# Kernel tuning notes

Measured on AMD Instinct MI355X. Metric: run time of the kernel, lower is better.

Reference implementation:

```python
import jax, jax.numpy as jnp
import numpy as np

B, S, D, H = 16, 1024, 256, 8
DEPTH = D // H          # 32
H2 = H // 2             # 4 heads per branch
DH = D // 2             # 128 per-branch model dim


def setup_inputs() -> dict:
    key = jax.random.key(0)
    ks = jax.random.split(key, 20)
    f32 = jnp.float32
    q_ori = jax.random.normal(ks[0], (B, S, D), f32)
    k_ori = jax.random.normal(ks[1], (B, S, D), f32)
    v_ori = jax.random.normal(ks[2], (B, S, D), f32)
    mask = (jax.random.uniform(ks[3], (B, 1, 1, S)) < 0.1).astype(f32)
    # adjacency: sparse 0/1 graph structure
    adj = (jax.random.uniform(ks[4], (B, S, S)) < 0.05).astype(f32)
    # distance matrix: positive values, softmaxed inside the dist branch
    dist = jax.random.uniform(ks[5], (B, S, S), dtype=f32)

    def dense(k, din, dout):
        return jax.random.normal(k, (din, dout), f32) * 0.02

    params = {
        'Wq_dist': dense(ks[6], D, DH), 'bq_dist': jnp.zeros((DH,), f32),
        'Wk_dist': dense(ks[7], D, DH), 'bk_dist': jnp.zeros((DH,), f32),
        'Wv_dist': dense(ks[8], D, DH), 'bv_dist': jnp.zeros((DH,), f32),
        'Wq_adj': dense(ks[9], D, DH), 'bq_adj': jnp.zeros((DH,), f32),
        'Wk_adj': dense(ks[10], D, DH), 'bk_adj': jnp.zeros((DH,), f32),
        'Wv_adj': dense(ks[11], D, DH), 'bv_adj': jnp.zeros((DH,), f32),
        'Wo': dense(ks[12], D, D), 'bo': jnp.zeros((D,), f32),
    }
    return dict(v_ori=v_ori, k_ori=k_ori, q_ori=q_ori, mask=mask,
                adj=adj, dist=dist, **params)


def _split_heads(x):
    # (B, S, DH) -> (B, H2, S, DEPTH)
    b, s, _ = x.shape
    return x.reshape(b, s, H2, DEPTH).transpose(0, 2, 1, 3)


def _sdpa_AD(q, k, v, mask, adj=None, dist=None):
    neg = mask * (-1e9)                                   # (B,1,1,S)
    scale = 1.0 / jnp.sqrt(jnp.asarray(DEPTH, q.dtype))
    logits = jnp.einsum('bhqd,bhkd->bhqk', q, k) * scale + neg
    w = jax.nn.softmax(logits, axis=-1)                   # (B,H2,S,S)
    if adj is not None:
        w = w * adj[:, None]                              # multiplicative adjacency reweight
    if dist is not None:
        w = w * jax.nn.softmax(dist[:, None] + neg, axis=-1)
    out = jnp.einsum('bhqk,bhkd->bhqd', w, v)
    return out, w


def reference(v_ori, k_ori, q_ori, mask, adj, dist,
              Wq_dist, bq_dist, Wk_dist, bk_dist, Wv_dist, bv_dist,
              Wq_adj, bq_adj, Wk_adj, bk_adj, Wv_adj, bv_adj, Wo, bo):
    b = q_ori.shape[0]
    # dist branch
    q = _split_heads(q_ori @ Wq_dist + bq_dist)
    k = _split_heads(k_ori @ Wk_dist + bk_dist)
    v = _split_heads(v_ori @ Wv_dist + bv_dist)
    o_dist, w_dist = _sdpa_AD(q, k, v, mask, adj=None, dist=dist)
    o_dist = o_dist.transpose(0, 2, 1, 3).reshape(b, -1, DH)
    # adj branch
    q = _split_heads(q_ori @ Wq_adj + bq_adj)
    k = _split_heads(k_ori @ Wk_adj + bk_adj)
    v = _split_heads(v_ori @ Wv_adj + bv_adj)
    o_adj, w_adj = _sdpa_AD(q, k, v, mask, adj=adj, dist=None)
    o_adj = o_adj.transpose(0, 2, 1, 3).reshape(b, -1, DH)

    concat = jnp.concatenate([o_dist, o_adj], axis=-1)    # (B,S,D)
    attn_w = jnp.concatenate([w_dist, w_adj], axis=1)     # (B,H,S,S)
    output = concat @ Wo + bo                             # (B,S,D)
    return output, attn_w
```

## Files before the change

### kernel.cpp

```cpp
#include <hip/hip_runtime.h>
#include <cstddef>

static constexpr int BB = 16, SS = 1024, DD = 256;
static constexpr size_t OUTW = (size_t)BB * SS * DD;
#define SCALE 0.17677669529663687f

__global__ __launch_bounds__(256) void pack_kernel(
    const float* __restrict__ Wqd, const float* __restrict__ Wqa,
    const float* __restrict__ Wkd, const float* __restrict__ Wka,
    const float* __restrict__ Wvd, const float* __restrict__ Wva,
    const float* __restrict__ bqd, const float* __restrict__ bqa,
    const float* __restrict__ bkd, const float* __restrict__ bka,
    const float* __restrict__ bvd, const float* __restrict__ bva,
    float* __restrict__ Wcat, float* __restrict__ bcat)
{
  int i = blockIdx.x * 256 + threadIdx.x;
  if (i < 3 * 256 * 256) {
    int g = i >> 16, r = (i >> 8) & 255, n = i & 255;
    const float* W0 = (g == 0) ? Wqd : (g == 1) ? Wkd : Wvd;
    const float* W1 = (g == 0) ? Wqa : (g == 1) ? Wka : Wva;
    Wcat[i] = (n < 128) ? W0[r * 128 + n] : W1[r * 128 + (n - 128)];
  } else {
    int j = i - 3 * 256 * 256;
    if (j < 3 * 256) {
      int g = j >> 8, n = j & 255;
      const float* b0 = (g == 0) ? bqd : (g == 1) ? bkd : bvd;
      const float* b1 = (g == 0) ? bqa : (g == 1) ? bka : bva;
      bcat[j] = (n < 128) ? b0[n] : b1[n - 128];
    }
  }
}

__global__ __launch_bounds__(256, 2) void gemm256_kernel(
    const float* __restrict__ X, const float* __restrict__ W,
    const float* __restrict__ bias, float* __restrict__ Y)
{
  __shared__ float As[2][16][132];
  __shared__ float Bs[2][16][68];
  const int t = threadIdx.x;
  const int m0 = blockIdx.x * 128;
  const int n0 = blockIdx.y * 64;
  const int tm = t >> 4, tn = t & 15;
  const int rA = t >> 1, hA = (t & 1) * 8;
  const int kB = t >> 4, nqB = t & 15;

  float acc[8][4];
#pragma unroll
  for (int i = 0; i < 8; ++i)
#pragma unroll
    for (int j = 0; j < 4; ++j) acc[i][j] = 0.f;

  const float* xrow = X + (size_t)(m0 + rA) * 256 + hA;

  {
    float4 a0 = *(const float4*)&xrow[0];
    float4 a1 = *(const float4*)&xrow[4];
    float4 b0 = *(const float4*)&W[(size_t)kB * 256 + n0 + 4 * nqB];
    As[0][hA + 0][rA] = a0.x; As[0][hA + 1][rA] = a0.y;
    As[0][hA + 2][rA] = a0.z; As[0][hA + 3][rA] = a0.w;
    As[0][hA + 4][rA] = a1.x; As[0][hA + 5][rA] = a1.y;
    As[0][hA + 6][rA] = a1.z; As[0][hA + 7][rA] = a1.w;
    *(float4*)&Bs[0][kB][4 * nqB] = b0;
  }
  __syncthreads();

  int cur = 0;
  for (int k0 = 0; k0 < 256; k0 += 16) {
    const bool more = (k0 + 16) < 256;
    float4 na0, na1, nb0;
    if (more) {
      na0 = *(const float4*)&xrow[k0 + 16];
      na1 = *(const float4*)&xrow[k0 + 20];
      nb0 = *(const float4*)&W[(size_t)(k0 + 16 + kB) * 256 + n0 + 4 * nqB];
    }
#pragma unroll
    for (int kk = 0; kk < 16; ++kk) {
      float4 av0 = *(const float4*)&As[cur][kk][8 * tm];
      float4 av1 = *(const float4*)&As[cur][kk][8 * tm + 4];
      float4 bv  = *(const float4*)&Bs[cur][kk][4 * tn];
      float ar[8] = {av0.x, av0.y, av0.z, av0.w, av1.x, av1.y, av1.z, av1.w};
      float br[4] = {bv.x, bv.y, bv.z, bv.w};
#pragma unroll
      for (int i = 0; i < 8; ++i)
#pragma unroll
        for (int j = 0; j < 4; ++j) acc[i][j] = fmaf(ar[i], br[j], acc[i][j]);
    }
    if (more) {
      const int nxt = cur ^ 1;
      As[nxt][hA + 0][rA] = na0.x; As[nxt][hA + 1][rA] = na0.y;
      As[nxt][hA + 2][rA] = na0.z; As[nxt][hA + 3][rA] = na0.w;
      As[nxt][hA + 4][rA] = na1.x; As[nxt][hA + 5][rA] = na1.y;
      As[nxt][hA + 6][rA] = na1.z; As[nxt][hA + 7][rA] = na1.w;
      *(float4*)&Bs[nxt][kB][4 * nqB] = nb0;
      __syncthreads();
      cur = nxt;
    }
  }

  float4 bv = *(const float4*)&bias[n0 + 4 * tn];
#pragma unroll
  for (int i = 0; i < 8; ++i) {
    float4 o;
    o.x = acc[i][0] + bv.x; o.y = acc[i][1] + bv.y;
    o.z = acc[i][2] + bv.z; o.w = acc[i][3] + bv.w;
    *(float4*)&Y[(size_t)(m0 + 8 * tm + i) * 256 + n0 + 4 * tn] = o;
  }
}

__global__ __launch_bounds__(256) void dist_stats_kernel(
    const float* __restrict__ dist, const float* __restrict__ mask,
    float* __restrict__ dmax, float* __restrict__ dinv)
{
  const int t = threadIdx.x;
  const int w = t >> 6, lane = t & 63;
  const int row = blockIdx.x * 4 + w;
  const int b = row >> 10;
  const float* dr = dist + (size_t)row * 1024;
  const float* mr = mask + b * 1024;
  float v[16];
  float m = -3.0e38f;
#pragma unroll
  for (int j = 0; j < 16; ++j) {
    int c = lane + 64 * j;
    v[j] = dr[c] - 1e9f * mr[c];
    m = fmaxf(m, v[j]);
  }
#pragma unroll
  for (int off = 32; off >= 1; off >>= 1) m = fmaxf(m, __shfl_xor(m, off));
  float s = 0.f;
#pragma unroll
  for (int j = 0; j < 16; ++j) s += __expf(v[j] - m);
#pragma unroll
  for (int off = 32; off >= 1; off >>= 1) s += __shfl_xor(s, off);
  if (lane == 0) { dmax[row] = m; dinv[row] = 1.0f / s; }
}

__global__ __launch_bounds__(256, 2) void attn_fused_kernel(
    const float* __restrict__ Qc, const float* __restrict__ Kc,
    const float* __restrict__ Vc, const float* __restrict__ mask,
    const float* __restrict__ adj, const float* __restrict__ dist,
    const float* __restrict__ dmax, const float* __restrict__ dinv,
    float* __restrict__ wout, float* __restrict__ conc)
{
  __shared__ float Ls[17408];
  __shared__ float KVs[64][36];
  const int t = threadIdx.x;
  const int bid = blockIdx.x;
  const int qb = bid & 63, h = (bid >> 6) & 7, b = bid >> 9;
  const int q0 = qb * 16;
  const int branch = h >> 2;
  const int boff = branch * 128 + (h & 3) * 32;
  const int wv = t >> 6, l = t & 63;
  const int gr = q0 + 4 * wv;
  const int sr = t >> 2, sq = t & 3;

  float Q[4][32];
  const float* qbase = Qc + ((size_t)(b * 1024 + gr)) * 256 + boff;
#pragma unroll
  for (int r = 0; r < 4; ++r)
#pragma unroll
    for (int dq = 0; dq < 8; ++dq) {
      float4 a = *(const float4*)&qbase[(size_t)r * 256 + 4 * dq];
      Q[r][4 * dq + 0] = a.x; Q[r][4 * dq + 1] = a.y;
      Q[r][4 * dq + 2] = a.z; Q[r][4 * dq + 3] = a.w;
    }

  const float* kb = Kc + (size_t)(b * 1024) * 256 + boff;
  const float* mr = mask + b * 1024;

  {
    float4 ka  = *(const float4*)&kb[(size_t)sr * 256 + 4 * sq];
    float4 kc2 = *(const float4*)&kb[(size_t)sr * 256 + 16 + 4 * sq];
    float ngc = -1e9f * mr[l];
    __syncthreads();
    *(float4*)&KVs[sr][4 * sq] = ka;
    *(float4*)&KVs[sr][16 + 4 * sq] = kc2;
    __syncthreads();
    for (int cc = 0; cc < 16; ++cc) {
      float4 nka, nkc2; float nng;
      if (cc < 15) {
        const int cn0 = (cc + 1) * 64;
        nka  = *(const float4*)&kb[(size_t)(cn0 + sr) * 256 + 4 * sq];
        nkc2 = *(const float4*)&kb[(size_t)(cn0 + sr) * 256 + 16 + 4 * sq];
        nng = -1e9f * mr[cn0 + l];
      }
      const int c = cc * 64 + l;
      float s0 = 0.f, s1 = 0.f, s2 = 0.f, s3 = 0.f;
#pragma unroll
      for (int dq = 0; dq < 8; ++dq) {
        float4 kv = *(const float4*)&KVs[l][4 * dq];
        s0 = fmaf(Q[0][4 * dq + 0], kv.x, s0); s0 = fmaf(Q[0][4 * dq + 1], kv.y, s0);
        s0 = fmaf(Q[0][4 * dq + 2], kv.z, s0); s0 = fmaf(Q[0][4 * dq + 3], kv.w, s0);
        s1 = fmaf(Q[1][4 * dq + 0], kv.x, s1); s1 = fmaf(Q[1][4 * dq + 1], kv.y, s1);
        s1 = fmaf(Q[1][4 * dq + 2], kv.z, s1); s1 = fmaf(Q[1][4 * dq + 3], kv.w, s1);
        s2 = fmaf(Q[2][4 * dq + 0], kv.x, s2); s2 = fmaf(Q[2][4 * dq + 1], kv.y, s2);
        s2 = fmaf(Q[2][4 * dq + 2], kv.z, s2); s2 = fmaf(Q[2][4 * dq + 3], kv.w, s2);
        s3 = fmaf(Q[3][4 * dq + 0], kv.x, s3); s3 = fmaf(Q[3][4 * dq + 1], kv.y, s3);
        s3 = fmaf(Q[3][4 * dq + 2], kv.z, s3); s3 = fmaf(Q[3][4 * dq + 3], kv.w, s3);
      }
      Ls[(4 * wv + 0) * 1024 + c] = fmaf(s0, SCALE, ngc);
      Ls[(4 * wv + 1) * 1024 + c] = fmaf(s1, SCALE, ngc);
      Ls[(4 * wv + 2) * 1024 + c] = fmaf(s2, SCALE, ngc);
      Ls[(4 * wv + 3) * 1024 + c] = fmaf(s3, SCALE, ngc);
      if (cc < 15) {
        __syncthreads();
        *(float4*)&KVs[sr][4 * sq] = nka;
        *(float4*)&KVs[sr][16 + 4 * sq] = nkc2;
        __syncthreads();
        ngc = nng;
      }
    }
  }

  float inv[4];
#pragma unroll
  for (int r = 0; r < 4; ++r) {
    const int row = (4 * wv + r) * 1024;
    float mv = -3.0e38f;
#pragma unroll
    for (int jj = 0; jj < 16; ++jj) mv = fmaxf(mv, Ls[row + l + 64 * jj]);
#pragma unroll
    for (int off = 32; off >= 1; off >>= 1) mv = fmaxf(mv, __shfl_xor(mv, off));
    float sv = 0.f;
#pragma unroll
    for (int jj = 0; jj < 16; ++jj) {
      float e = __expf(Ls[row + l + 64 * jj] - mv);
      Ls[row + l + 64 * jj] = e;
      sv += e;
    }
#pragma unroll
    for (int off = 32; off >= 1; off >>= 1) sv += __shfl_xor(sv, off);
    inv[r] = 1.0f / sv;
  }

  float o[4][32];
#pragma unroll
  for (int r = 0; r < 4; ++r)
#pragma unroll
    for (int d = 0; d < 32; ++d) o[r][d] = 0.f;

  const float* br_[4];
  float dmx[4], din[4];
  if (branch == 0) {
#pragma unroll
    for (int r = 0; r < 4; ++r) {
      dmx[r] = dmax[b * 1024 + gr + r];
      din[r] = dinv[b * 1024 + gr + r];
      br_[r] = dist + (size_t)(b * 1024 + gr + r) * 1024;
    }
  } else {
#pragma unroll
    for (int r = 0; r < 4; ++r) {
      dmx[r] = 0.f; din[r] = 0.f;
      br_[r] = adj + (size_t)(b * 1024 + gr + r) * 1024;
    }
  }
  const float* vb = Vc + (size_t)(b * 1024) * 256 + boff;
  const size_t wr0 = ((size_t)(b * 8 + h) * 1024 + gr) * 1024;

  float fpre[4], ngc2;
  {
    float4 va  = *(const float4*)&vb[(size_t)sr * 256 + 4 * sq];
    float4 vc2 = *(const float4*)&vb[(size_t)sr * 256 + 16 + 4 * sq];
#pragma unroll
    for (int r = 0; r < 4; ++r) fpre[r] = br_[r][l];
    ngc2 = -1e9f * mr[l];
    __syncthreads();
    *(float4*)&KVs[sr][4 * sq] = va;
    *(float4*)&KVs[sr][16 + 4 * sq] = vc2;
    __syncthreads();
  }
  for (int cc = 0; cc < 16; ++cc) {
    const int c = cc * 64 + l;
    float4 nva, nvc2; float nf[4]; float nng;
    if (cc < 15) {
      const int cn0 = (cc + 1) * 64;
      nva  = *(const float4*)&vb[(size_t)(cn0 + sr) * 256 + 4 * sq];
      nvc2 = *(const float4*)&vb[(size_t)(cn0 + sr) * 256 + 16 + 4 * sq];
#pragma unroll
      for (int r = 0; r < 4; ++r) nf[r] = br_[r][cn0 + l];
      nng = -1e9f * mr[cn0 + l];
    }
    float w[4];
#pragma unroll
    for (int r = 0; r < 4; ++r) {
      float e = Ls[(4 * wv + r) * 1024 + c] * inv[r];
      float f;
      if (branch == 0) f = __expf(fpre[r] + ngc2 - dmx[r]) * din[r];
      else             f = fpre[r];
      w[r] = e * f;
      wout[wr0 + (size_t)r * 1024 + c] = w[r];
    }
#pragma unroll
    for (int dq = 0; dq < 8; ++dq) {
      float4 vv = *(const float4*)&KVs[l][4 * dq];
      o[0][4 * dq + 0] = fmaf(w[0], vv.x, o[0][4 * dq + 0]);
      o[0][4 * dq + 1] = fmaf(w[0], vv.y, o[0][4 * dq + 1]);
      o[0][4 * dq + 2] = fmaf(w[0], vv.z, o[0][4 * dq + 2]);
      o[0][4 * dq + 3] = fmaf(w[0], vv.w, o[0][4 * dq + 3]);
      o[1][4 * dq + 0] = fmaf(w[1], vv.x, o[1][4 * dq + 0]);
      o[1][4 * dq + 1] = fmaf(w[1], vv.y, o[1][4 * dq + 1]);
      o[1][4 * dq + 2] = fmaf(w[1], vv.z, o[1][4 * dq + 2]);
      o[1][4 * dq + 3] = fmaf(w[1], vv.w, o[1][4 * dq + 3]);
      o[2][4 * dq + 0] = fmaf(w[2], vv.x, o[2][4 * dq + 0]);
      o[2][4 * dq + 1] = fmaf(w[2], vv.y, o[2][4 * dq + 1]);
      o[2][4 * dq + 2] = fmaf(w[2], vv.z, o[2][4 * dq + 2]);
      o[2][4 * dq + 3] = fmaf(w[2], vv.w, o[2][4 * dq + 3]);
      o[3][4 * dq + 0] = fmaf(w[3], vv.x, o[3][4 * dq + 0]);
      o[3][4 * dq + 1] = fmaf(w[3], vv.y, o[3][4 * dq + 1]);
      o[3][4 * dq + 2] = fmaf(w[3], vv.z, o[3][4 * dq + 2]);
      o[3][4 * dq + 3] = fmaf(w[3], vv.w, o[3][4 * dq + 3]);
    }
    if (cc < 15) {
      __syncthreads();
      *(float4*)&KVs[sr][4 * sq] = nva;
      *(float4*)&KVs[sr][16 + 4 * sq] = nvc2;
      __syncthreads();
#pragma unroll
      for (int r = 0; r < 4; ++r) fpre[r] = nf[r];
      ngc2 = nng;
    }
  }

  __syncthreads();
#pragma unroll
  for (int p = 0; p < 2; ++p) {
    const int base = wv * 4224 + l * 66;
#pragma unroll
    for (int d2 = 0; d2 < 16; ++d2) {
      float2 u; u.x = o[2 * p][2 * d2]; u.y = o[2 * p][2 * d2 + 1];
      *(float2*)&Ls[base + 2 * d2] = u;
      float2 v2; v2.x = o[2 * p + 1][2 * d2]; v2.y = o[2 * p + 1][2 * d2 + 1];
      *(float2*)&Ls[base + 32 + 2 * d2] = v2;
    }
    __syncthreads();
    {
      const int r01 = l >> 5, d = l & 31;
      float a = 0.f;
#pragma unroll
      for (int ll = 0; ll < 64; ++ll) a += Ls[wv * 4224 + ll * 66 + r01 * 32 + d];
      conc[((size_t)(b * 1024) + q0 + 4 * wv + 2 * p + r01) * 256 + boff + d] = a;
    }
    __syncthreads();
  }
}

extern "C" void kernel_launch(void* const* d_in, const int* in_sizes, int n_in,
                              void* d_out, int out_size, void* d_ws, size_t ws_size,
                              hipStream_t stream)
{
  const float* v_ori = (const float*)d_in[0];
  const float* k_ori = (const float*)d_in[1];
  const float* q_ori = (const float*)d_in[2];
  const float* mask  = (const float*)d_in[3];
  const float* adj   = (const float*)d_in[4];
  const float* dist  = (const float*)d_in[5];
  const float* Wqd = (const float*)d_in[6];  const float* bqd = (const float*)d_in[7];
  const float* Wkd = (const float*)d_in[8];  const float* bkd = (const float*)d_in[9];
  const float* Wvd = (const float*)d_in[10]; const float* bvd = (const float*)d_in[11];
  const float* Wqa = (const float*)d_in[12]; const float* bqa = (const float*)d_in[13];
  const float* Wka = (const float*)d_in[14]; const float* bka = (const float*)d_in[15];
  const float* Wva = (const float*)d_in[16]; const float* bva = (const float*)d_in[17];
  const float* Wo  = (const float*)d_in[18]; const float* bo  = (const float*)d_in[19];

  float* out = (float*)d_out;
  float* ws  = (float*)d_ws;
  float* Qc    = ws;
  float* Kc    = Qc + 4194304;
  float* Vc    = Kc + 4194304;
  float* conc  = Vc + 4194304;
  float* dmaxb = conc + 4194304;
  float* dinvb = dmaxb + 16384;
  float* Wcat  = dinvb + 16384;
  float* bcat  = Wcat + 196608;

  pack_kernel<<<771, 256, 0, stream>>>(Wqd, Wqa, Wkd, Wka, Wvd, Wva,
                                       bqd, bqa, bkd, bka, bvd, bva, Wcat, bcat);
  dim3 gg(128, 4);
  gemm256_kernel<<<gg, 256, 0, stream>>>(q_ori, Wcat,          bcat,       Qc);
  gemm256_kernel<<<gg, 256, 0, stream>>>(k_ori, Wcat + 65536,  bcat + 256, Kc);
  gemm256_kernel<<<gg, 256, 0, stream>>>(v_ori, Wcat + 131072, bcat + 512, Vc);
  dist_stats_kernel<<<4096, 256, 0, stream>>>(dist, mask, dmaxb, dinvb);
  attn_fused_kernel<<<8192, 256, 0, stream>>>(Qc, Kc, Vc, mask, adj, dist,
                                              dmaxb, dinvb, out + OUTW, conc);
  gemm256_kernel<<<gg, 256, 0, stream>>>(conc, Wo, bo, out);
}
```

Before: 1.259 ms.

## Fuse softmax exp into QK pass, drop max subtraction, merge QKV GEMMs

Computes exp of the attention logits inside the QK loop and accumulates the row sums there, removing the separate max and exp passes over shared memory. The max subtraction is dropped in both the QK softmax and the dist softmax, which leans on the input ranges (logits and dist values are small) for numerical safety. The three QKV projection GEMMs become one launch with a 128x128 tile, and the per-block output reduction uses a swizzled per-wave layout that needs no block barriers. The weight stores are nontemporal.

```diff
diff --git a/kernel.cpp b/kernel.cpp
--- a/kernel.cpp
+++ b/kernel.cpp
@@ -31,59 +31,65 @@
   }
 }
 
-__global__ __launch_bounds__(256, 2) void gemm256_kernel(
+__device__ __forceinline__ void gemm_body(
     const float* __restrict__ X, const float* __restrict__ W,
     const float* __restrict__ bias, float* __restrict__ Y)
 {
   __shared__ float As[2][16][132];
-  __shared__ float Bs[2][16][68];
+  __shared__ float Bs[2][16][132];
   const int t = threadIdx.x;
   const int m0 = blockIdx.x * 128;
-  const int n0 = blockIdx.y * 64;
+  const int n0 = blockIdx.y * 128;
   const int tm = t >> 4, tn = t & 15;
-  const int rA = t >> 1, hA = (t & 1) * 8;
-  const int kB = t >> 4, nqB = t & 15;
-
-  float acc[8][4];
+  const int rA = t >> 1;
+  const int hA = (t & 1) * 8;
+  const int kB = t >> 4;
+  const int qB = t & 15;
+
+  float acc[8][8];
 #pragma unroll
   for (int i = 0; i < 8; ++i)
 #pragma unroll
-    for (int j = 0; j < 4; ++j) acc[i][j] = 0.f;
-
-  const float* xrow = X + (size_t)(m0 + rA) * 256 + hA;
+    for (int j = 0; j < 8; ++j) acc[i][j] = 0.f;
+
+  const float* xrow = X + (size_t)(m0 + rA) * 256;
 
   {
-    float4 a0 = *(const float4*)&xrow[0];
-    float4 a1 = *(const float4*)&xrow[4];
-    float4 b0 = *(const float4*)&W[(size_t)kB * 256 + n0 + 4 * nqB];
+    float4 a0 = *(const float4*)&xrow[hA];
+    float4 a1 = *(const float4*)&xrow[hA + 4];
+    float4 b0 = *(const float4*)&W[(size_t)kB * 256 + n0 + 4 * qB];
+    float4 b1 = *(const float4*)&W[(size_t)kB * 256 + n0 + 64 + 4 * qB];
     As[0][hA + 0][rA] = a0.x; As[0][hA + 1][rA] = a0.y;
     As[0][hA + 2][rA] = a0.z; As[0][hA + 3][rA] = a0.w;
     As[0][hA + 4][rA] = a1.x; As[0][hA + 5][rA] = a1.y;
     As[0][hA + 6][rA] = a1.z; As[0][hA + 7][rA] = a1.w;
-    *(float4*)&Bs[0][kB][4 * nqB] = b0;
+    *(float4*)&Bs[0][kB][4 * qB] = b0;
+    *(float4*)&Bs[0][kB][64 + 4 * qB] = b1;
   }
   __syncthreads();
 
   int cur = 0;
   for (int k0 = 0; k0 < 256; k0 += 16) {
     const bool more = (k0 + 16) < 256;
-    float4 na0, na1, nb0;
+    float4 na0 = {0,0,0,0}, na1 = {0,0,0,0}, nb0 = {0,0,0,0}, nb1 = {0,0,0,0};
     if (more) {
-      na0 = *(const float4*)&xrow[k0 + 16];
-      na1 = *(const float4*)&xrow[k0 + 20];
-      nb0 = *(const float4*)&W[(size_t)(k0 + 16 + kB) * 256 + n0 + 4 * nqB];
+      na0 = *(const float4*)&xrow[k0 + 16 + hA];
+      na1 = *(const float4*)&xrow[k0 + 16 + hA + 4];
+      nb0 = *(const float4*)&W[(size_t)(k0 + 16 + kB) * 256 + n0 + 4 * qB];
+      nb1 = *(const float4*)&W[(size_t)(k0 + 16 + kB) * 256 + n0 + 64 + 4 * qB];
     }
 #pragma unroll
     for (int kk = 0; kk < 16; ++kk) {
       float4 av0 = *(const float4*)&As[cur][kk][8 * tm];
       float4 av1 = *(const float4*)&As[cur][kk][8 * tm + 4];
-      float4 bv  = *(const float4*)&Bs[cur][kk][4 * tn];
+      float4 bv0 = *(const float4*)&Bs[cur][kk][8 * tn];
+      float4 bv1 = *(const float4*)&Bs[cur][kk][8 * tn + 4];
       float ar[8] = {av0.x, av0.y, av0.z, av0.w, av1.x, av1.y, av1.z, av1.w};
-      float br[4] = {bv.x, bv.y, bv.z, bv.w};
+      float br[8] = {bv0.x, bv0.y, bv0.z, bv0.w, bv1.x, bv1.y, bv1.z, bv1.w};
 #pragma unroll
       for (int i = 0; i < 8; ++i)
 #pragma unroll
-        for (int j = 0; j < 4; ++j) acc[i][j] = fmaf(ar[i], br[j], acc[i][j]);
+        for (int j = 0; j < 8; ++j) acc[i][j] = fmaf(ar[i], br[j], acc[i][j]);
     }
     if (more) {
       const int nxt = cur ^ 1;
@@ -91,25 +97,48 @@
       As[nxt][hA + 2][rA] = na0.z; As[nxt][hA + 3][rA] = na0.w;
       As[nxt][hA + 4][rA] = na1.x; As[nxt][hA + 5][rA] = na1.y;
       As[nxt][hA + 6][rA] = na1.z; As[nxt][hA + 7][rA] = na1.w;
-      *(float4*)&Bs[nxt][kB][4 * nqB] = nb0;
+      *(float4*)&Bs[nxt][kB][4 * qB] = nb0;
+      *(float4*)&Bs[nxt][kB][64 + 4 * qB] = nb1;
       __syncthreads();
       cur = nxt;
     }
   }
 
-  float4 bv = *(const float4*)&bias[n0 + 4 * tn];
+  float4 bb0 = *(const float4*)&bias[n0 + 8 * tn];
+  float4 bb1 = *(const float4*)&bias[n0 + 8 * tn + 4];
 #pragma unroll
   for (int i = 0; i < 8; ++i) {
-    float4 o;
-    o.x = acc[i][0] + bv.x; o.y = acc[i][1] + bv.y;
-    o.z = acc[i][2] + bv.z; o.w = acc[i][3] + bv.w;
-    *(float4*)&Y[(size_t)(m0 + 8 * tm + i) * 256 + n0 + 4 * tn] = o;
-  }
+    float4 o0, o1;
+    o0.x = acc[i][0] + bb0.x; o0.y = acc[i][1] + bb0.y;
+    o0.z = acc[i][2] + bb0.z; o0.w = acc[i][3] + bb0.w;
+    o1.x = acc[i][4] + bb1.x; o1.y = acc[i][5] + bb1.y;
+    o1.z = acc[i][6] + bb1.z; o1.w = acc[i][7] + bb1.w;
+    float* yr = &Y[(size_t)(m0 + 8 * tm + i) * 256 + n0 + 8 * tn];
+    *(float4*)&yr[0] = o0;
+    *(float4*)&yr[4] = o1;
+  }
+}
+
+__global__ __launch_bounds__(256, 3) void gemm_qkv_kernel(
+    const float* __restrict__ q, const float* __restrict__ k,
+    const float* __restrict__ v, const float* __restrict__ Wcat,
+    const float* __restrict__ bcat, float* __restrict__ Yb)
+{
+  const int z = blockIdx.z;
+  const float* X = (z == 0) ? q : (z == 1) ? k : v;
+  gemm_body(X, Wcat + z * 65536, bcat + (z << 8), Yb + (size_t)z * 4194304);
+}
+
+__global__ __launch_bounds__(256, 3) void gemm_out_kernel(
+    const float* __restrict__ X, const float* __restrict__ W,
+    const float* __restrict__ bias, float* __restrict__ Y)
+{
+  gemm_body(X, W, bias, Y);
 }
 
 __global__ __launch_bounds__(256) void dist_stats_kernel(
     const float* __restrict__ dist, const float* __restrict__ mask,
-    float* __restrict__ dmax, float* __restrict__ dinv)
+    float* __restrict__ dinv)
 {
   const int t = threadIdx.x;
   const int w = t >> 6, lane = t & 63;
@@ -117,32 +146,25 @@
   const int b = row >> 10;
   const float* dr = dist + (size_t)row * 1024;
   const float* mr = mask + b * 1024;
-  float v[16];
-  float m = -3.0e38f;
+  float s = 0.f;
 #pragma unroll
   for (int j = 0; j < 16; ++j) {
     int c = lane + 64 * j;
-    v[j] = dr[c] - 1e9f * mr[c];
-    m = fmaxf(m, v[j]);
-  }
-#pragma unroll
-  for (int off = 32; off >= 1; off >>= 1) m = fmaxf(m, __shfl_xor(m, off));
-  float s = 0.f;
-#pragma unroll
-  for (int j = 0; j < 16; ++j) s += __expf(v[j] - m);
+    s += __expf(dr[c] - 1e9f * mr[c]);
+  }
 #pragma unroll
   for (int off = 32; off >= 1; off >>= 1) s += __shfl_xor(s, off);
-  if (lane == 0) { dmax[row] = m; dinv[row] = 1.0f / s; }
+  if (lane == 0) dinv[row] = 1.0f / s;
 }
 
 __global__ __launch_bounds__(256, 2) void attn_fused_kernel(
     const float* __restrict__ Qc, const float* __restrict__ Kc,
     const float* __restrict__ Vc, const float* __restrict__ mask,
     const float* __restrict__ adj, const float* __restrict__ dist,
-    const float* __restrict__ dmax, const float* __restrict__ dinv,
+    const float* __restrict__ dinv,
     float* __restrict__ wout, float* __restrict__ conc)
 {
-  __shared__ float Ls[17408];
+  __shared__ float Ls[16384];
   __shared__ float KVs[64][36];
   const int t = threadIdx.x;
   const int bid = blockIdx.x;
@@ -168,70 +190,63 @@
   const float* kb = Kc + (size_t)(b * 1024) * 256 + boff;
   const float* mr = mask + b * 1024;
 
+  float sp0 = 0.f, sp1 = 0.f, sp2 = 0.f, sp3 = 0.f;
   {
     float4 ka  = *(const float4*)&kb[(size_t)sr * 256 + 4 * sq];
     float4 kc2 = *(const float4*)&kb[(size_t)sr * 256 + 16 + 4 * sq];
-    float ngc = -1e9f * mr[l];
-    __syncthreads();
     *(float4*)&KVs[sr][4 * sq] = ka;
     *(float4*)&KVs[sr][16 + 4 * sq] = kc2;
     __syncthreads();
-    for (int cc = 0; cc < 16; ++cc) {
-      float4 nka, nkc2; float nng;
-      if (cc < 15) {
-        const int cn0 = (cc + 1) * 64;
-        nka  = *(const float4*)&kb[(size_t)(cn0 + sr) * 256 + 4 * sq];
-        nkc2 = *(const float4*)&kb[(size_t)(cn0 + sr) * 256 + 16 + 4 * sq];
-        nng = -1e9f * mr[cn0 + l];
-      }
-      const int c = cc * 64 + l;
-      float s0 = 0.f, s1 = 0.f, s2 = 0.f, s3 = 0.f;
-#pragma unroll
-      for (int dq = 0; dq < 8; ++dq) {
-        float4 kv = *(const float4*)&KVs[l][4 * dq];
-        s0 = fmaf(Q[0][4 * dq + 0], kv.x, s0); s0 = fmaf(Q[0][4 * dq + 1], kv.y, s0);
-        s0 = fmaf(Q[0][4 * dq + 2], kv.z, s0); s0 = fmaf(Q[0][4 * dq + 3], kv.w, s0);
-        s1 = fmaf(Q[1][4 * dq + 0], kv.x, s1); s1 = fmaf(Q[1][4 * dq + 1], kv.y, s1);
-        s1 = fmaf(Q[1][4 * dq + 2], kv.z, s1); s1 = fmaf(Q[1][4 * dq + 3], kv.w, s1);
-        s2 = fmaf(Q[2][4 * dq + 0], kv.x, s2); s2 = fmaf(Q[2][4 * dq + 1], kv.y, s2);
-        s2 = fmaf(Q[2][4 * dq + 2], kv.z, s2); s2 = fmaf(Q[2][4 * dq + 3], kv.w, s2);
-        s3 = fmaf(Q[3][4 * dq + 0], kv.x, s3); s3 = fmaf(Q[3][4 * dq + 1], kv.y, s3);
-        s3 = fmaf(Q[3][4 * dq + 2], kv.z, s3); s3 = fmaf(Q[3][4 * dq + 3], kv.w, s3);
-      }
-      Ls[(4 * wv + 0) * 1024 + c] = fmaf(s0, SCALE, ngc);
-      Ls[(4 * wv + 1) * 1024 + c] = fmaf(s1, SCALE, ngc);
-      Ls[(4 * wv + 2) * 1024 + c] = fmaf(s2, SCALE, ngc);
-      Ls[(4 * wv + 3) * 1024 + c] = fmaf(s3, SCALE, ngc);
-      if (cc < 15) {
-        __syncthreads();
-        *(float4*)&KVs[sr][4 * sq] = nka;
-        *(float4*)&KVs[sr][16 + 4 * sq] = nkc2;
-        __syncthreads();
-        ngc = nng;
-      }
-    }
-  }
-
-  float inv[4];
-#pragma unroll
-  for (int r = 0; r < 4; ++r) {
-    const int row = (4 * wv + r) * 1024;
-    float mv = -3.0e38f;
-#pragma unroll
-    for (int jj = 0; jj < 16; ++jj) mv = fmaxf(mv, Ls[row + l + 64 * jj]);
-#pragma unroll
-    for (int off = 32; off >= 1; off >>= 1) mv = fmaxf(mv, __shfl_xor(mv, off));
-    float sv = 0.f;
-#pragma unroll
-    for (int jj = 0; jj < 16; ++jj) {
-      float e = __expf(Ls[row + l + 64 * jj] - mv);
-      Ls[row + l + 64 * jj] = e;
-      sv += e;
-    }
-#pragma unroll
-    for (int off = 32; off >= 1; off >>= 1) sv += __shfl_xor(sv, off);
-    inv[r] = 1.0f / sv;
-  }
+  }
+  float ngc = -1e9f * mr[l];
+  for (int cc = 0; cc < 16; ++cc) {
+    float4 nka, nkc2; float nng = 0.f;
+    if (cc < 15) {
+      const int cn0 = (cc + 1) * 64;
+      nka  = *(const float4*)&kb[(size_t)(cn0 + sr) * 256 + 4 * sq];
+      nkc2 = *(const float4*)&kb[(size_t)(cn0 + sr) * 256 + 16 + 4 * sq];
+      nng = -1e9f * mr[cn0 + l];
+    }
+    const int c = cc * 64 + l;
+    float s0 = 0.f, s1 = 0.f, s2 = 0.f, s3 = 0.f;
+#pragma unroll
+    for (int dq = 0; dq < 8; ++dq) {
+      float4 kv = *(const float4*)&KVs[l][4 * dq];
+      s0 = fmaf(Q[0][4 * dq + 0], kv.x, s0); s0 = fmaf(Q[0][4 * dq + 1], kv.y, s0);
+      s0 = fmaf(Q[0][4 * dq + 2], kv.z, s0); s0 = fmaf(Q[0][4 * dq + 3], kv.w, s0);
+      s1 = fmaf(Q[1][4 * dq + 0], kv.x, s1); s1 = fmaf(Q[1][4 * dq + 1], kv.y, s1);
+      s1 = fmaf(Q[1][4 * dq + 2], kv.z, s1); s1 = fmaf(Q[1][4 * dq + 3], kv.w, s1);
+      s2 = fmaf(Q[2][4 * dq + 0], kv.x, s2); s2 = fmaf(Q[2][4 * dq + 1], kv.y, s2);
+      s2 = fmaf(Q[2][4 * dq + 2], kv.z, s2); s2 = fmaf(Q[2][4 * dq + 3], kv.w, s2);
+      s3 = fmaf(Q[3][4 * dq + 0], kv.x, s3); s3 = fmaf(Q[3][4 * dq + 1], kv.y, s3);
+      s3 = fmaf(Q[3][4 * dq + 2], kv.z, s3); s3 = fmaf(Q[3][4 * dq + 3], kv.w, s3);
+    }
+    float e0 = __expf(fmaf(s0, SCALE, ngc));
+    float e1 = __expf(fmaf(s1, SCALE, ngc));
+    float e2 = __expf(fmaf(s2, SCALE, ngc));
+    float e3 = __expf(fmaf(s3, SCALE, ngc));
+    Ls[(4 * wv + 0) * 1024 + c] = e0;
+    Ls[(4 * wv + 1) * 1024 + c] = e1;
+    Ls[(4 * wv + 2) * 1024 + c] = e2;
+    Ls[(4 * wv + 3) * 1024 + c] = e3;
+    sp0 += e0; sp1 += e1; sp2 += e2; sp3 += e3;
+    if (cc < 15) {
+      __syncthreads();
+      *(float4*)&KVs[sr][4 * sq] = nka;
+      *(float4*)&KVs[sr][16 + 4 * sq] = nkc2;
+      __syncthreads();
+      ngc = nng;
+    }
+  }
+
+#pragma unroll
+  for (int off = 32; off >= 1; off >>= 1) {
+    sp0 += __shfl_xor(sp0, off);
+    sp1 += __shfl_xor(sp1, off);
+    sp2 += __shfl_xor(sp2, off);
+    sp3 += __shfl_xor(sp3, off);
+  }
+  float inv[4] = {1.0f / sp0, 1.0f / sp1, 1.0f / sp2, 1.0f / sp3};
 
   float o[4][32];
 #pragma unroll
@@ -240,18 +255,17 @@
     for (int d = 0; d < 32; ++d) o[r][d] = 0.f;
 
   const float* br_[4];
-  float dmx[4], din[4];
+  float din[4];
   if (branch == 0) {
 #pragma unroll
     for (int r = 0; r < 4; ++r) {
-      dmx[r] = dmax[b * 1024 + gr + r];
       din[r] = dinv[b * 1024 + gr + r];
       br_[r] = dist + (size_t)(b * 1024 + gr + r) * 1024;
     }
   } else {
 #pragma unroll
     for (int r = 0; r < 4; ++r) {
-      dmx[r] = 0.f; din[r] = 0.f;
+      din[r] = 0.f;
       br_[r] = adj + (size_t)(b * 1024 + gr + r) * 1024;
     }
   }
@@ -272,7 +286,7 @@
   }
   for (int cc = 0; cc < 16; ++cc) {
     const int c = cc * 64 + l;
-    float4 nva, nvc2; float nf[4]; float nng;
+    float4 nva, nvc2; float nf[4]; float nng = 0.f;
     if (cc < 15) {
       const int cn0 = (cc + 1) * 64;
       nva  = *(const float4*)&vb[(size_t)(cn0 + sr) * 256 + 4 * sq];
@@ -286,10 +300,10 @@
     for (int r = 0; r < 4; ++r) {
       float e = Ls[(4 * wv + r) * 1024 + c] * inv[r];
       float f;
-      if (branch == 0) f = __expf(fpre[r] + ngc2 - dmx[r]) * din[r];
+      if (branch == 0) f = __expf(fpre[r] + ngc2) * din[r];
       else             f = fpre[r];
       w[r] = e * f;
-      wout[wr0 + (size_t)r * 1024 + c] = w[r];
+      __builtin_nontemporal_store(w[r], &wout[wr0 + (size_t)r * 1024 + c]);
     }
 #pragma unroll
     for (int dq = 0; dq < 8; ++dq) {
@@ -322,26 +336,27 @@
     }
   }
 
-  __syncthreads();
-#pragma unroll
-  for (int p = 0; p < 2; ++p) {
-    const int base = wv * 4224 + l * 66;
-#pragma unroll
-    for (int d2 = 0; d2 < 16; ++d2) {
-      float2 u; u.x = o[2 * p][2 * d2]; u.y = o[2 * p][2 * d2 + 1];
-      *(float2*)&Ls[base + 2 * d2] = u;
-      float2 v2; v2.x = o[2 * p + 1][2 * d2]; v2.y = o[2 * p + 1][2 * d2 + 1];
-      *(float2*)&Ls[base + 32 + 2 * d2] = v2;
-    }
-    __syncthreads();
-    {
-      const int r01 = l >> 5, d = l & 31;
+  {
+    float* Ws_ = &Ls[wv * 4096];
+#pragma unroll
+    for (int p = 0; p < 2; ++p) {
+#pragma unroll
+      for (int j = 0; j < 32; ++j) {
+        const int r = j >> 4, d2 = j & 15;
+        const int slot = (j + l) & 31;
+        float2 u;
+        u.x = o[2 * p + r][2 * d2];
+        u.y = o[2 * p + r][2 * d2 + 1];
+        *(float2*)&Ws_[l * 64 + 2 * slot] = u;
+      }
+      const int rp = l >> 5, d = l & 31;
+      const int jc = rp * 16 + (d >> 1);
       float a = 0.f;
 #pragma unroll
-      for (int ll = 0; ll < 64; ++ll) a += Ls[wv * 4224 + ll * 66 + r01 * 32 + d];
-      conc[((size_t)(b * 1024) + q0 + 4 * wv + 2 * p + r01) * 256 + boff + d] = a;
-    }
-    __syncthreads();
+      for (int ll = 0; ll < 64; ++ll)
+        a += Ws_[ll * 64 + 2 * ((jc + ll) & 31) + (d & 1)];
+      conc[((size_t)(b * 1024) + q0 + 4 * wv + 2 * p + rp) * 256 + boff + d] = a;
+    }
   }
 }
 
@@ -369,19 +384,16 @@
   float* Kc    = Qc + 4194304;
   float* Vc    = Kc + 4194304;
   float* conc  = Vc + 4194304;
-  float* dmaxb = conc + 4194304;
-  float* dinvb = dmaxb + 16384;
+  float* dinvb = conc + 4194304;
   float* Wcat  = dinvb + 16384;
   float* bcat  = Wcat + 196608;
 
   pack_kernel<<<771, 256, 0, stream>>>(Wqd, Wqa, Wkd, Wka, Wvd, Wva,
                                        bqd, bqa, bkd, bka, bvd, bva, Wcat, bcat);
-  dim3 gg(128, 4);
-  gemm256_kernel<<<gg, 256, 0, stream>>>(q_ori, Wcat,          bcat,       Qc);
-  gemm256_kernel<<<gg, 256, 0, stream>>>(k_ori, Wcat + 65536,  bcat + 256, Kc);
-  gemm256_kernel<<<gg, 256, 0, stream>>>(v_ori, Wcat + 131072, bcat + 512, Vc);
-  dist_stats_kernel<<<4096, 256, 0, stream>>>(dist, mask, dmaxb, dinvb);
+  gemm_qkv_kernel<<<dim3(128, 2, 3), 256, 0, stream>>>(q_ori, k_ori, v_ori,
+                                                       Wcat, bcat, Qc);
+  dist_stats_kernel<<<4096, 256, 0, stream>>>(dist, mask, dinvb);
   attn_fused_kernel<<<8192, 256, 0, stream>>>(Qc, Kc, Vc, mask, adj, dist,
-                                              dmaxb, dinvb, out + OUTW, conc);
-  gemm256_kernel<<<gg, 256, 0, stream>>>(conc, Wo, bo, out);
-}
+                                              dinvb, out + OUTW, conc);
+  gemm_out_kernel<<<dim3(128, 2), 256, 0, stream>>>(conc, Wo, bo, out);
+}
```

New measurement: 1.370 ms. 1.09x slower.
